# Performance work log

Measured on AMD Instinct MI355X. Metric: run time of the kernel, lower is better.

## Reference

```python
import jax, jax.numpy as jnp
import numpy as np

N, D = 16384, 256

def setup_inputs() -> dict:
    key = jax.random.key(0)
    k1, k2 = jax.random.split(key)
    image_features = jax.random.normal(k1, (N, D), dtype=jnp.float32)
    text_features = jax.random.normal(k2, (N, D), dtype=jnp.float32)
    logit_scale = jnp.float32(14.285714)  # exp(log(1/0.07)), typical CLIP temperature
    targets = jnp.arange(N, dtype=jnp.int64)
    return {"image_features": image_features, "text_features": text_features,
            "logit_scale": logit_scale, "targets": targets}

def _cross_entropy(logits, targets):
    # mean over rows of -log_softmax(logits)[i, targets[i]]
    logp = jax.nn.log_softmax(logits, axis=-1)
    return -jnp.mean(jnp.take_along_axis(logp, targets[:, None], axis=-1))

def reference(image_features, text_features, logit_scale, targets):
    logits = logit_scale * (image_features @ text_features.T)  # [N, N]
    image_loss = _cross_entropy(logits, targets)
    text_loss = _cross_entropy(logits.T, targets)
    return (image_loss + text_loss) / 2.0
```

## Files before the change

kernel.cpp:

```cpp
#include <hip/hip_runtime.h>

#define N_ 16384
#define D_ 256
#define LOG2E 1.4426950408889634f
#define HEXP2(x) __builtin_amdgcn_exp2f(x)

typedef __attribute__((ext_vector_type(8))) short short8;
typedef __attribute__((ext_vector_type(16))) float floatx16;

typedef __attribute__((address_space(1))) const unsigned int gu32_t;
typedef __attribute__((address_space(3))) unsigned int lu32_t;

__device__ __forceinline__ void async16(const void* g, void* l) {
  __builtin_amdgcn_global_load_lds((gu32_t*)g, (lu32_t*)l, 16, 0, 0);
}

__device__ __forceinline__ unsigned short f2bf(float x) {
  unsigned int u = __float_as_uint(x);
  u += 0x7fffu + ((u >> 16) & 1u);
  return (unsigned short)(u >> 16);
}

__global__ void prep_pack(const float* __restrict__ img, const float* __restrict__ txt,
                          const float* __restrict__ ls, short* __restrict__ PA,
                          short* __restrict__ PB, float* __restrict__ diag2,
                          float* __restrict__ out) {
  const int tid = threadIdx.x;
  const int t = blockIdx.x * 1024 + tid;
  const int m = tid & 31, h = (tid >> 5) & 1, ks = (tid >> 6) & 15;
  const int G = blockIdx.x;
  const int row = G * 32 + m, col = ks * 16 + h * 8;
  const float s2 = ls[0] * LOG2E;
  const float4* sa = (const float4*)(img + (size_t)row * D_ + col);
  const float4* sb = (const float4*)(txt + (size_t)row * D_ + col);
  float4 a0 = sa[0], a1 = sa[1];
  float4 b0 = sb[0], b1 = sb[1];
  short8 oa, ob;
  oa[0] = (short)f2bf(a0.x * s2); oa[1] = (short)f2bf(a0.y * s2);
  oa[2] = (short)f2bf(a0.z * s2); oa[3] = (short)f2bf(a0.w * s2);
  oa[4] = (short)f2bf(a1.x * s2); oa[5] = (short)f2bf(a1.y * s2);
  oa[6] = (short)f2bf(a1.z * s2); oa[7] = (short)f2bf(a1.w * s2);
  ob[0] = (short)f2bf(b0.x); ob[1] = (short)f2bf(b0.y);
  ob[2] = (short)f2bf(b0.z); ob[3] = (short)f2bf(b0.w);
  ob[4] = (short)f2bf(b1.x); ob[5] = (short)f2bf(b1.y);
  ob[6] = (short)f2bf(b1.z); ob[7] = (short)f2bf(b1.w);
  ((short8*)PA)[t] = oa;
  ((short8*)PB)[t] = ob;

  float d = a0.x * b0.x + a0.y * b0.y + a0.z * b0.z + a0.w * b0.w
          + a1.x * b1.x + a1.y * b1.y + a1.z * b1.z + a1.w * b1.w;
  __shared__ float red[32][33];
  red[tid >> 5][m] = d;
  __syncthreads();
  if (tid < 32) {
    float s = 0.f;
    #pragma unroll
    for (int q = 0; q < 32; ++q) s += red[q][tid];
    diag2[G * 32 + tid] = s * s2;
  }
  if (t == 0) out[0] = 0.f;
}

__global__ __launch_bounds__(256, 2)
void gemm_stats(const short* __restrict__ PA, const short* __restrict__ PB,
                float2* __restrict__ pR, float2* __restrict__ pC) {
  __shared__ __align__(16) char smem[73728];
  float* rowbuf  = (float*)(smem + 32768);
  float2* colbuf = (float2*)(smem + 71680);

  const int tid = threadIdx.x, lane = tid & 63, wv = tid >> 6;
  const int wr = wv >> 1, wc = wv & 1;
  const int m = lane & 31, h = lane >> 5;
  const int stripe = blockIdx.x, by = blockIdx.y;

  short8 areg[2][16];
  #pragma unroll
  for (int g = 0; g < 2; ++g)
    #pragma unroll
    for (int ks = 0; ks < 16; ++ks)
      areg[g][ks] = *(const short8*)(PA +
          ((size_t)((stripe * 4 + wr * 2 + g) * 16 + ks)) * 512 + lane * 8);
  asm volatile("s_waitcnt vmcnt(0)" ::: "memory");

  floatx16 acc[2][2];

  auto issue = [&](int jj2, int c2, int bufsel) {
    const short* base = PB + ((size_t)((by * 64 + jj2 * 4) * 16) + c2 * 4 + wv) * 512 + lane * 8;
    char* dst = smem + bufsel * 16384 + wv * 1024;
    #pragma unroll
    for (int ct = 0; ct < 4; ++ct)
      async16(base + (size_t)ct * 8192, dst + ct * 4096);
  };
  auto compute = [&](int c, int bufsel) {
    char* base = smem + bufsel * 16384 + lane * 16;
    #pragma unroll
    for (int ksl = 0; ksl < 4; ++ksl) {
      short8 b0 = *(const short8*)(base + ((wc * 2 + 0) * 4 + ksl) * 1024);
      short8 b1 = *(const short8*)(base + ((wc * 2 + 1) * 4 + ksl) * 1024);
      int ks = c * 4 + ksl;
      acc[0][0] = __builtin_amdgcn_mfma_f32_32x32x16_bf16(areg[0][ks], b0, acc[0][0], 0, 0, 0);
      acc[1][0] = __builtin_amdgcn_mfma_f32_32x32x16_bf16(areg[1][ks], b0, acc[1][0], 0, 0, 0);
      acc[0][1] = __builtin_amdgcn_mfma_f32_32x32x16_bf16(areg[0][ks], b1, acc[0][1], 0, 0, 0);
      acc[1][1] = __builtin_amdgcn_mfma_f32_32x32x16_bf16(areg[1][ks], b1, acc[1][1], 0, 0, 0);
    }
  };

  issue(0, 0, 0);
  issue(0, 1, 1);

  float Mr = -3.0e38f, Sr = 0.f;

  for (int jj = 0; jj < 16; ++jj) {
    #pragma unroll
    for (int rt = 0; rt < 2; ++rt)
      #pragma unroll
      for (int ctl = 0; ctl < 2; ++ctl)
        #pragma unroll
        for (int r = 0; r < 16; ++r) acc[rt][ctl][r] = 0.f;

    #pragma unroll
    for (int c = 0; c < 4; ++c) {
      if (jj == 15 && c == 3) { asm volatile("s_waitcnt vmcnt(0)" ::: "memory"); }
      else                    { asm volatile("s_waitcnt vmcnt(4)" ::: "memory"); }
      __builtin_amdgcn_s_barrier();
      asm volatile("" ::: "memory");
      compute(c, c & 1);
      asm volatile("" ::: "memory");
      __builtin_amdgcn_s_barrier();
      asm volatile("" ::: "memory");
      int nc = c + 2;
      int jj2 = jj + (nc >> 2);
      if (jj2 < 16) issue(jj2, nc & 3, nc & 1);
    }

    float vm[4];
    #pragma unroll
    for (int q = 0; q < 4; ++q) {
      float a01 = fmaxf(acc[q >> 1][q & 1][0],  acc[q >> 1][q & 1][1]);
      float a23 = fmaxf(acc[q >> 1][q & 1][2],  acc[q >> 1][q & 1][3]);
      float a45 = fmaxf(acc[q >> 1][q & 1][4],  acc[q >> 1][q & 1][5]);
      float a67 = fmaxf(acc[q >> 1][q & 1][6],  acc[q >> 1][q & 1][7]);
      float a89 = fmaxf(acc[q >> 1][q & 1][8],  acc[q >> 1][q & 1][9]);
      float aab = fmaxf(acc[q >> 1][q & 1][10], acc[q >> 1][q & 1][11]);
      float acd = fmaxf(acc[q >> 1][q & 1][12], acc[q >> 1][q & 1][13]);
      float aef = fmaxf(acc[q >> 1][q & 1][14], acc[q >> 1][q & 1][15]);
      vm[q] = fmaxf(fmaxf(fmaxf(a01, a23), fmaxf(a45, a67)),
                    fmaxf(fmaxf(a89, aab), fmaxf(acd, aef)));
    }
    float v = fmaxf(fmaxf(vm[0], vm[1]), fmaxf(vm[2], vm[3]));
    #pragma unroll
    for (int off = 1; off < 64; off <<= 1) v = fmaxf(v, __shfl_xor(v, off));
    float msub = v - 96.f;

    #pragma unroll
    for (int rt = 0; rt < 2; ++rt)
      #pragma unroll
      for (int ctl = 0; ctl < 2; ++ctl)
        #pragma unroll
        for (int r = 0; r < 16; ++r) acc[rt][ctl][r] = HEXP2(acc[rt][ctl][r] - msub);

    #pragma unroll
    for (int ctl = 0; ctl < 2; ++ctl) {
      float cp = 0.f;
      #pragma unroll
      for (int r = 0; r < 16; ++r) cp += acc[0][ctl][r] + acc[1][ctl][r];
      cp += __shfl_xor(cp, 32);
      if (h == 0) colbuf[wr * 128 + wc * 64 + ctl * 32 + m] = make_float2(msub, cp);
    }

    #pragma unroll
    for (int rt = 0; rt < 2; ++rt)
      #pragma unroll
      for (int rq = 0; rq < 4; ++rq) {
        float4 rp;
        rp.x = acc[rt][0][rq * 4 + 0] + acc[rt][1][rq * 4 + 0];
        rp.y = acc[rt][0][rq * 4 + 1] + acc[rt][1][rq * 4 + 1];
        rp.z = acc[rt][0][rq * 4 + 2] + acc[rt][1][rq * 4 + 2];
        rp.w = acc[rt][0][rq * 4 + 3] + acc[rt][1][rq * 4 + 3];
        *(float4*)&rowbuf[(wr * 64 + wc * 32 + m) * 76 + rt * 32 + rq * 8 + h * 4] = rp;
      }
    asm volatile("s_waitcnt lgkmcnt(0)" ::: "memory");
    __builtin_amdgcn_s_barrier();
    asm volatile("" ::: "memory");

    {
      float s = 0.f;
      #pragma unroll
      for (int k = 0; k < 32; ++k)
        s += rowbuf[(wr * 64 + h * 32 + k) * 76 + wc * 32 + m];
      s += __shfl_xor(s, 32);
      if (s > 0.f) {
        if (msub > Mr) { Sr = Sr * HEXP2(Mr - msub) + s; Mr = msub; }
        else           { Sr += s * HEXP2(msub - Mr); }
      }
    }
    if (tid < 128) {
      float2 c0 = colbuf[tid], c1 = colbuf[128 + tid];
      float M = -3.0e38f, L = 0.f;
      if (c0.y > 0.f) { M = c0.x; L = c0.y; }
      if (c1.y > 0.f) {
        if (c1.x > M) { L = L * HEXP2(M - c1.x) + c1.y; M = c1.x; }
        else          { L += c1.y * HEXP2(c1.x - M); }
      }
      pC[(size_t)stripe * N_ + by * 2048 + jj * 128 + tid] = make_float2(M, L);
    }
    asm volatile("s_waitcnt lgkmcnt(0)" ::: "memory");
    __builtin_amdgcn_s_barrier();
    asm volatile("" ::: "memory");
  }

  if (h == 0)
    pR[(size_t)by * N_ + stripe * 128 + wr * 64 + wc * 32 + m] = make_float2(Mr, Sr);
}

__global__ void merge_kernel(const float2* __restrict__ pR, const float2* __restrict__ pC,
                             const float* __restrict__ diag2, float* __restrict__ out) {
  auto mrg = [](float& M, float& L, float2 w) {
    if (w.y > 0.f) {
      if (w.x > M) { L = L * exp2f(M - w.x) + w.y; M = w.x; }
      else         { L += w.y * exp2f(w.x - M); }
    }
  };
  int idx = blockIdx.x * 256 + threadIdx.x;
  float M = -3.0e38f, L = 0.f;
  int i;
  if (idx < N_) {
    i = idx;
    #pragma unroll
    for (int g = 0; g < 8; ++g) mrg(M, L, pR[(size_t)g * N_ + i]);
  } else {
    i = idx - N_;
    float M1 = -3.0e38f, L1 = 0.f, M2 = -3.0e38f, L2 = 0.f, M3 = -3.0e38f, L3 = 0.f;
    #pragma unroll 4
    for (int s = 0; s < 128; s += 4) {
      mrg(M,  L,  pC[(size_t)(s + 0) * N_ + i]);
      mrg(M1, L1, pC[(size_t)(s + 1) * N_ + i]);
      mrg(M2, L2, pC[(size_t)(s + 2) * N_ + i]);
      mrg(M3, L3, pC[(size_t)(s + 3) * N_ + i]);
    }
    mrg(M, L, make_float2(M1, L1));
    mrg(M, L, make_float2(M2, L2));
    mrg(M, L, make_float2(M3, L3));
  }
  float val = (M + log2f(fmaxf(L, 1e-45f))) - diag2[i];

  __shared__ float red[256];
  red[threadIdx.x] = val;
  __syncthreads();
  #pragma unroll
  for (int s = 128; s > 0; s >>= 1) {
    if (threadIdx.x < s) red[threadIdx.x] += red[threadIdx.x + s];
    __syncthreads();
  }
  if (threadIdx.x == 0)
    atomicAdd(out, red[0] * (0.69314718055994531f / 32768.0f));
}

extern "C" void kernel_launch(void* const* d_in, const int* in_sizes, int n_in,
                              void* d_out, int out_size, void* d_ws, size_t ws_size,
                              hipStream_t stream) {
  const float* img = (const float*)d_in[0];
  const float* txt = (const float*)d_in[1];
  const float* ls  = (const float*)d_in[2];
  float* out = (float*)d_out;

  char* ws = (char*)d_ws;
  short* PA    = (short*)(ws);
  short* PB    = (short*)(ws + 8388608);
  float* diag2 = (float*)(ws + 16777216);
  float2* pR   = (float2*)(ws + 16843008);
  float2* pC   = (float2*)(ws + 17891584);

  hipLaunchKernelGGL(prep_pack, dim3(512), dim3(1024), 0, stream, img, txt, ls, PA, PB, diag2, out);
  hipLaunchKernelGGL(gemm_stats, dim3(128, 8), dim3(256), 0, stream, PA, PB, pR, pC);
  hipLaunchKernelGGL(merge_kernel, dim3(2 * N_ / 256), dim3(256), 0, stream, pR, pC, diag2, out);
}
```

Baseline: 273.8 us.

## Give each wave private B staging buffers and reduce row sums via shuffles

Each wave now loads its own copy of the B tiles it needs into a private double-buffered LDS region. This removes the two block-wide barriers around every k-chunk compute, at the cost of duplicate global loads: waves sharing a column half fetch the same data. The row-sum path now pre-reduces across lanes with xor shuffles and writes a compact buffer that is read back with float4 loads, replacing the 32-iteration strided LDS sum. LDS use grows slightly, and the extra global traffic could pressure bandwidth or L2.

New measurement: 329.7 us. 1.2x slower.

```diff
diff --git a/kernel.cpp b/kernel.cpp
--- a/kernel.cpp
+++ b/kernel.cpp
@@ -64,9 +64,9 @@
 __global__ __launch_bounds__(256, 2)
 void gemm_stats(const short* __restrict__ PA, const short* __restrict__ PB,
                 float2* __restrict__ pR, float2* __restrict__ pC) {
-  __shared__ __align__(16) char smem[73728];
-  float* rowbuf  = (float*)(smem + 32768);
-  float2* colbuf = (float2*)(smem + 71680);
+  __shared__ __align__(16) char smem[77824];
+  float* rowbuf2 = (float*)(smem + 65536);
+  float2* colbuf = (float2*)(smem + 75776);
 
   const int tid = threadIdx.x, lane = tid & 63, wv = tid >> 6;
   const int wr = wv >> 1, wc = wv & 1;
@@ -84,19 +84,23 @@
 
   floatx16 acc[2][2];
 
-  auto issue = [&](int jj2, int c2, int bufsel) {
-    const short* base = PB + ((size_t)((by * 64 + jj2 * 4) * 16) + c2 * 4 + wv) * 512 + lane * 8;
-    char* dst = smem + bufsel * 16384 + wv * 1024;
-    #pragma unroll
-    for (int ct = 0; ct < 4; ++ct)
-      async16(base + (size_t)ct * 8192, dst + ct * 4096);
+  auto issue = [&](int n, int bufsel) {
+    int jj2 = n >> 2, c2 = n & 3;
+    const short* base = PB +
+        ((size_t)((by * 64 + jj2 * 4 + wc * 2) * 16) + c2 * 4) * 512 + lane * 8;
+    char* dst = smem + wv * 16384 + bufsel * 8192;
+    #pragma unroll
+    for (int ctl = 0; ctl < 2; ++ctl)
+      #pragma unroll
+      for (int ksl = 0; ksl < 4; ++ksl)
+        async16(base + (size_t)(ctl * 16 + ksl) * 512, dst + (ctl * 4 + ksl) * 1024);
   };
   auto compute = [&](int c, int bufsel) {
-    char* base = smem + bufsel * 16384 + lane * 16;
+    char* base = smem + wv * 16384 + bufsel * 8192 + lane * 16;
     #pragma unroll
     for (int ksl = 0; ksl < 4; ++ksl) {
-      short8 b0 = *(const short8*)(base + ((wc * 2 + 0) * 4 + ksl) * 1024);
-      short8 b1 = *(const short8*)(base + ((wc * 2 + 1) * 4 + ksl) * 1024);
+      short8 b0 = *(const short8*)(base + (0 * 4 + ksl) * 1024);
+      short8 b1 = *(const short8*)(base + (1 * 4 + ksl) * 1024);
       int ks = c * 4 + ksl;
       acc[0][0] = __builtin_amdgcn_mfma_f32_32x32x16_bf16(areg[0][ks], b0, acc[0][0], 0, 0, 0);
       acc[1][0] = __builtin_amdgcn_mfma_f32_32x32x16_bf16(areg[1][ks], b0, acc[1][0], 0, 0, 0);
@@ -105,8 +109,8 @@
     }
   };
 
-  issue(0, 0, 0);
-  issue(0, 1, 1);
+  issue(0, 0);
+  issue(1, 1);
 
   float Mr = -3.0e38f, Sr = 0.f;
 
@@ -120,17 +124,12 @@
 
     #pragma unroll
     for (int c = 0; c < 4; ++c) {
-      if (jj == 15 && c == 3) { asm volatile("s_waitcnt vmcnt(0)" ::: "memory"); }
-      else                    { asm volatile("s_waitcnt vmcnt(4)" ::: "memory"); }
-      __builtin_amdgcn_s_barrier();
-      asm volatile("" ::: "memory");
+      int n = jj * 4 + c;
+      if (n == 63) { asm volatile("s_waitcnt vmcnt(0)" ::: "memory"); }
+      else         { asm volatile("s_waitcnt vmcnt(8)" ::: "memory"); }
       compute(c, c & 1);
-      asm volatile("" ::: "memory");
-      __builtin_amdgcn_s_barrier();
-      asm volatile("" ::: "memory");
-      int nc = c + 2;
-      int jj2 = jj + (nc >> 2);
-      if (jj2 < 16) issue(jj2, nc & 3, nc & 1);
+      asm volatile("s_waitcnt lgkmcnt(0)" ::: "memory");
+      if (n + 2 < 64) issue(n + 2, c & 1);
     }
 
     float vm[4];
@@ -168,27 +167,36 @@
       if (h == 0) colbuf[wr * 128 + wc * 64 + ctl * 32 + m] = make_float2(msub, cp);
     }
 
-    #pragma unroll
-    for (int rt = 0; rt < 2; ++rt)
-      #pragma unroll
-      for (int rq = 0; rq < 4; ++rq) {
-        float4 rp;
-        rp.x = acc[rt][0][rq * 4 + 0] + acc[rt][1][rq * 4 + 0];
-        rp.y = acc[rt][0][rq * 4 + 1] + acc[rt][1][rq * 4 + 1];
-        rp.z = acc[rt][0][rq * 4 + 2] + acc[rt][1][rq * 4 + 2];
-        rp.w = acc[rt][0][rq * 4 + 3] + acc[rt][1][rq * 4 + 3];
-        *(float4*)&rowbuf[(wr * 64 + wc * 32 + m) * 76 + rt * 32 + rq * 8 + h * 4] = rp;
+    float rp[2][16];
+    #pragma unroll
+    for (int rt = 0; rt < 2; ++rt)
+      #pragma unroll
+      for (int r = 0; r < 16; ++r) {
+        float x = acc[rt][0][r] + acc[rt][1][r];
+        x += __shfl_xor(x, 8);
+        x += __shfl_xor(x, 16);
+        rp[rt][r] = x;
       }
+    #pragma unroll
+    for (int rt = 0; rt < 2; ++rt)
+      #pragma unroll
+      for (int r = 0; r < 16; ++r)
+        if ((m >> 3) == rt)
+          rowbuf2[(size_t)(wr * 64 + rt * 32 + (r & 3) + 8 * (r >> 2) + 4 * h) * 20 +
+                  wc * 8 + (m & 7)] = rp[rt][r];
+
     asm volatile("s_waitcnt lgkmcnt(0)" ::: "memory");
     __builtin_amdgcn_s_barrier();
     asm volatile("" ::: "memory");
 
     {
-      float s = 0.f;
-      #pragma unroll
-      for (int k = 0; k < 32; ++k)
-        s += rowbuf[(wr * 64 + h * 32 + k) * 76 + wc * 32 + m];
-      s += __shfl_xor(s, 32);
+      const float* rb = rowbuf2 + (size_t)(wr * 64 + wc * 32 + m) * 20;
+      float4 q0 = *(const float4*)(rb + 0);
+      float4 q1 = *(const float4*)(rb + 4);
+      float4 q2 = *(const float4*)(rb + 8);
+      float4 q3 = *(const float4*)(rb + 12);
+      float s = ((q0.x + q0.y) + (q0.z + q0.w)) + ((q1.x + q1.y) + (q1.z + q1.w))
+              + ((q2.x + q2.y) + (q2.z + q2.w)) + ((q3.x + q3.y) + (q3.z + q3.w));
       if (s > 0.f) {
         if (msub > Mr) { Sr = Sr * HEXP2(Mr - msub) + s; Mr = msub; }
         else           { Sr += s * HEXP2(msub - Mr); }
```

## Coalesce prep_pack reads via LDS transpose and remap gemm block order

Applied to the files above, without the earlier changes.

The pack kernel now reads each block's 32 rows contiguously from the fp32 inputs and transposes through XOR-swizzled shared memory before writing the MFMA-tiled bf16 layout. This replaces the old strided global reads. Separately, the GEMM kernel remaps its linear block index so consecutive workgroups land on different stripe/column combinations, which changes L2 and cache locality across XCDs. The extra LDS round trip and a barrier add some latency to the small prep kernel.

Measured after the change: 286.4 us. +4.6%, slower.

```diff
diff --git a/kernel.cpp b/kernel.cpp
--- a/kernel.cpp
+++ b/kernel.cpp
@@ -25,16 +25,19 @@
                           const float* __restrict__ ls, short* __restrict__ PA,
                           short* __restrict__ PB, float* __restrict__ diag2,
                           float* __restrict__ out) {
-  const int tid = threadIdx.x;
-  const int t = blockIdx.x * 1024 + tid;
-  const int m = tid & 31, h = (tid >> 5) & 1, ks = (tid >> 6) & 15;
+  __shared__ __align__(16) short8 lds_a[1024];
+  __shared__ __align__(16) short8 lds_b[1024];
+  __shared__ float red2[32][33];
+  const int t = threadIdx.x;
   const int G = blockIdx.x;
-  const int row = G * 32 + m, col = ks * 16 + h * 8;
+  const int row = t >> 5, kq = t & 31;
   const float s2 = ls[0] * LOG2E;
-  const float4* sa = (const float4*)(img + (size_t)row * D_ + col);
-  const float4* sb = (const float4*)(txt + (size_t)row * D_ + col);
-  float4 a0 = sa[0], a1 = sa[1];
-  float4 b0 = sb[0], b1 = sb[1];
+
+  const float4* sa = (const float4*)(img + (size_t)G * 8192);
+  const float4* sb = (const float4*)(txt + (size_t)G * 8192);
+  float4 a0 = sa[2 * t], a1 = sa[2 * t + 1];
+  float4 b0 = sb[2 * t], b1 = sb[2 * t + 1];
+
   short8 oa, ob;
   oa[0] = (short)f2bf(a0.x * s2); oa[1] = (short)f2bf(a0.y * s2);
   oa[2] = (short)f2bf(a0.z * s2); oa[3] = (short)f2bf(a0.w * s2);
@@ -44,21 +47,28 @@
   ob[2] = (short)f2bf(b0.z); ob[3] = (short)f2bf(b0.w);
   ob[4] = (short)f2bf(b1.x); ob[5] = (short)f2bf(b1.y);
   ob[6] = (short)f2bf(b1.z); ob[7] = (short)f2bf(b1.w);
-  ((short8*)PA)[t] = oa;
-  ((short8*)PB)[t] = ob;
+
+  const int pos = (kq >> 1) * 64 + (kq & 1) * 32 + row;
+  const int spos = pos ^ ((pos >> 6) & 7);
+  lds_a[spos] = oa;
+  lds_b[spos] = ob;
 
   float d = a0.x * b0.x + a0.y * b0.y + a0.z * b0.z + a0.w * b0.w
           + a1.x * b1.x + a1.y * b1.y + a1.z * b1.z + a1.w * b1.w;
-  __shared__ float red[32][33];
-  red[tid >> 5][m] = d;
+  red2[kq][row] = d;
   __syncthreads();
-  if (tid < 32) {
+
+  const int rp = t ^ ((t >> 6) & 7);
+  ((short8*)PA)[(size_t)G * 1024 + t] = lds_a[rp];
+  ((short8*)PB)[(size_t)G * 1024 + t] = lds_b[rp];
+
+  if (t < 32) {
     float s = 0.f;
     #pragma unroll
-    for (int q = 0; q < 32; ++q) s += red[q][tid];
-    diag2[G * 32 + tid] = s * s2;
-  }
-  if (t == 0) out[0] = 0.f;
+    for (int q = 0; q < 32; ++q) s += red2[q][t];
+    diag2[G * 32 + t] = s * s2;
+  }
+  if (G == 0 && t == 0) out[0] = 0.f;
 }
 
 __global__ __launch_bounds__(256, 2)
@@ -71,7 +81,9 @@
   const int tid = threadIdx.x, lane = tid & 63, wv = tid >> 6;
   const int wr = wv >> 1, wc = wv & 1;
   const int m = lane & 31, h = lane >> 5;
-  const int stripe = blockIdx.x, by = blockIdx.y;
+  const int orig = blockIdx.x + blockIdx.y * 128;
+  const int swz = (orig & 7) * 128 + (orig >> 3);
+  const int stripe = swz & 127, by = swz >> 7;
 
   short8 areg[2][16];
   #pragma unroll
```
